# Kernel optimization log

Hardware: AMD Instinct MI355X
Metric: run time of the kernel (lower is better)

The kernel has to match this reference:

```python
import jax, jax.numpy as jnp
import numpy as np

D_MODEL = 512
NHEAD = 8
WINDOW = 64


def setup_inputs() -> dict:
    key = jax.random.key(0)
    ks = jax.random.split(key, 5)
    d = D_MODEL
    x = jax.random.normal(ks[0], (8, 2048, d), dtype=jnp.float32)
    # nn.MultiheadAttention params: packed in-proj [3d, d] + bias [3d], out-proj [d, d] + bias [d]
    scale = 1.0 / np.sqrt(d)
    in_proj_w = jax.random.normal(ks[1], (3 * d, d), dtype=jnp.float32) * scale
    in_proj_b = jnp.zeros((3 * d,), dtype=jnp.float32)
    out_proj_w = jax.random.normal(ks[2], (d, d), dtype=jnp.float32) * scale
    out_proj_b = jnp.zeros((d,), dtype=jnp.float32)
    return {"x": x, "in_proj_w": in_proj_w, "in_proj_b": in_proj_b,
            "out_proj_w": out_proj_w, "out_proj_b": out_proj_b}


def reference(x, in_proj_w, in_proj_b, out_proj_w, out_proj_b):
    B, L, d = x.shape
    H = NHEAD
    dh = d // H
    # packed qkv projection (torch Linear: x @ W.T + b)
    qkv = jnp.einsum('bld,ed->ble', x, in_proj_w) + in_proj_b  # [B, L, 3d]
    q, k, v = jnp.split(qkv, 3, axis=-1)
    # split heads -> [B, H, L, dh]
    def heads(t):
        return t.reshape(B, L, H, dh).transpose(0, 2, 1, 3)
    q, k, v = heads(q), heads(k), heads(v)
    scores = jnp.einsum('bhqd,bhkd->bhqk', q, k) / jnp.sqrt(jnp.float32(dh))
    # banded mask: positions with |i-j| > window are masked out
    idx = jnp.arange(L)
    band = jnp.abs(idx[None, :] - idx[:, None]) > WINDOW  # [L, L] bool
    scores = jnp.where(band[None, None, :, :], jnp.float32(-jnp.inf), scores)
    p = jax.nn.softmax(scores, axis=-1)
    out = jnp.einsum('bhqk,bhkd->bhqd', p, v)  # [B, H, L, dh]
    out = out.transpose(0, 2, 1, 3).reshape(B, L, d)
    return jnp.einsum('bld,ed->ble', out, out_proj_w) + out_proj_b
```

## Files before the change

kernel.cpp:

```cpp
#include <hip/hip_runtime.h>

typedef __bf16 bf16x8 __attribute__((ext_vector_type(8)));
typedef unsigned short u16;
typedef unsigned short u16x8 __attribute__((ext_vector_type(8)));
typedef float f32x4 __attribute__((ext_vector_type(4)));

#define L_SEQ 2048
#define NQT   (L_SEQ / 128)

__device__ __forceinline__ float bf2f(u16 x) {
    unsigned u = ((unsigned)x) << 16;
    return __builtin_bit_cast(float, u);
}
__device__ __forceinline__ u16 f2bf(float f) {
    unsigned u = __builtin_bit_cast(unsigned, f);
    u += 0x7FFFu + ((u >> 16) & 1u);
    return (u16)(u >> 16);
}

__device__ __forceinline__ void gload_lds16(const u16* g, u16* l) {
    __builtin_amdgcn_global_load_lds(
        (const __attribute__((address_space(1))) void*)g,
        (__attribute__((address_space(3))) void*)l, 16, 0, 0);
}

__global__ void cvt_all(const float* __restrict__ x, const float* __restrict__ wi,
                        const float* __restrict__ wo, u16* __restrict__ xo,
                        u16* __restrict__ wio, u16* __restrict__ woo,
                        int nx8, int nwi8, int nwo8) {
    int i = blockIdx.x * blockDim.x + threadIdx.x;
    const float* src; u16* dst;
    if (i < nx8) { src = x; dst = xo; }
    else if (i < nx8 + nwi8) { i -= nx8; src = wi; dst = wio; }
    else if (i < nx8 + nwi8 + nwo8) { i -= nx8 + nwi8; src = wo; dst = woo; }
    else return;
    const float4* p = reinterpret_cast<const float4*>(src) + (size_t)i * 2;
    const float4 a = p[0], b = p[1];
    u16x8 r;
    r[0] = f2bf(a.x); r[1] = f2bf(a.y); r[2] = f2bf(a.z); r[3] = f2bf(a.w);
    r[4] = f2bf(b.x); r[5] = f2bf(b.y); r[6] = f2bf(b.z); r[7] = f2bf(b.w);
    *(reinterpret_cast<u16x8*>(dst) + i) = r;
}

__launch_bounds__(512, 4)
__global__ void gemm_qkv(const u16* __restrict__ A, const u16* __restrict__ W,
                         const float* __restrict__ bias, u16* __restrict__ C,
                         int M, int N, int K) {
    __shared__ u16 As[3][256 * 32];
    __shared__ u16 Bs[3][128 * 32];

    const int tid   = threadIdx.x;
    const int lane  = tid & 63;
    const int wid   = tid >> 6;
    const int wm    = wid >> 1;
    const int wn    = wid & 1;
    const int row_l = lane & 15;
    const int grp   = lane >> 4;

    const int nwg  = gridDim.x * gridDim.y;
    const int hw   = blockIdx.y * gridDim.x + blockIdx.x;
    const int tile = (hw & 7) * (nwg >> 3) + (hw >> 3);
    const int m0 = (tile / gridDim.x) * 256;
    const int n0 = (tile % gridDim.x) * 128;

    const int srow = tid >> 2;
    const int scol = ((tid & 3) ^ ((tid >> 3) & 3)) * 8;
    const u16* gA = A + (size_t)(m0 + srow) * K + scol;
    const u16* gB = W + (size_t)(n0 + srow) * K + scol;

    f32x4 acc[4][4];
#pragma unroll
    for (int mi = 0; mi < 4; ++mi)
#pragma unroll
        for (int ni = 0; ni < 4; ++ni)
            acc[mi][ni] = (f32x4){0.f, 0.f, 0.f, 0.f};

    auto stage = [&](int buf, int kt) {
        gload_lds16(gA + (size_t)kt * 32,                   &As[buf][0]    + wid * 512);
        gload_lds16(gA + (size_t)128 * K + (size_t)kt * 32, &As[buf][4096] + wid * 512);
        gload_lds16(gB + (size_t)kt * 32,                   &Bs[buf][0]    + wid * 512);
    };

    const int rchunk = (grp ^ ((row_l >> 1) & 3)) * 8;

    const int NT = K >> 5;
    stage(0, 0);
    stage(1, 1);
    asm volatile("s_waitcnt vmcnt(3)" ::: "memory");
    __builtin_amdgcn_s_barrier();

    int buf = 0;
    for (int kt = 0; kt < NT; ++kt) {
        bf16x8 a[4], b[4];
#pragma unroll
        for (int mi = 0; mi < 4; ++mi)
            a[mi] = *reinterpret_cast<const bf16x8*>(
                &As[buf][(wm * 64 + mi * 16 + row_l) * 32 + rchunk]);
#pragma unroll
        for (int ni = 0; ni < 4; ++ni)
            b[ni] = *reinterpret_cast<const bf16x8*>(
                &Bs[buf][(wn * 64 + ni * 16 + row_l) * 32 + rchunk]);

        if (kt + 2 < NT) {
            int st = buf + 2; if (st >= 3) st -= 3;
            stage(st, kt + 2);
        }
        if (kt < NT - 2)       asm volatile("s_waitcnt vmcnt(3)" ::: "memory");
        else if (kt == NT - 2) asm volatile("s_waitcnt vmcnt(0)" ::: "memory");
        __builtin_amdgcn_s_barrier();
        asm volatile("s_waitcnt lgkmcnt(0)" ::: "memory");
        __builtin_amdgcn_sched_barrier(0);
        __builtin_amdgcn_s_setprio(1);
#pragma unroll
        for (int mi = 0; mi < 4; ++mi)
#pragma unroll
            for (int ni = 0; ni < 4; ++ni)
                acc[mi][ni] = __builtin_amdgcn_mfma_f32_16x16x32_bf16(a[mi], b[ni], acc[mi][ni], 0, 0, 0);
        __builtin_amdgcn_s_setprio(0);
        __builtin_amdgcn_s_barrier();
        buf = buf + 1; if (buf >= 3) buf = 0;
    }

#pragma unroll
    for (int ni = 0; ni < 4; ++ni) {
        const int col = n0 + wn * 64 + ni * 16 + row_l;
        const float bsf = bias[col];
#pragma unroll
        for (int mi = 0; mi < 4; ++mi) {
#pragma unroll
            for (int r = 0; r < 4; ++r) {
                const int rowm = m0 + wm * 64 + mi * 16 + grp * 4 + r;
                C[(size_t)rowm * N + col] = f2bf(acc[mi][ni][r] + bsf);
            }
        }
    }
}

template <bool OUT_BF16>
__launch_bounds__(256, 3)
__global__ void gemm_ring(const u16* __restrict__ A, const u16* __restrict__ W,
                          const float* __restrict__ bias, void* __restrict__ Cv,
                          int M, int N, int K) {
    __shared__ u16 As[3][128 * 32];
    __shared__ u16 Bs[3][128 * 32];

    const int tid   = threadIdx.x;
    const int lane  = tid & 63;
    const int wid   = tid >> 6;
    const int wm    = wid >> 1;
    const int wn    = wid & 1;
    const int row_l = lane & 15;
    const int grp   = lane >> 4;

    const int nwg  = gridDim.x * gridDim.y;
    const int hw   = blockIdx.y * gridDim.x + blockIdx.x;
    const int tile = (hw & 7) * (nwg >> 3) + (hw >> 3);
    const int m0 = (tile / gridDim.x) * 128;
    const int n0 = (tile % gridDim.x) * 128;

    const int srow = tid >> 2;
    const int scol = ((tid & 3) ^ ((tid >> 3) & 3)) * 8;
    const u16* gA = A + (size_t)(m0 + srow) * K + scol;
    const u16* gB = W + (size_t)(n0 + srow) * K + scol;

    f32x4 acc[4][4];
#pragma unroll
    for (int mi = 0; mi < 4; ++mi)
#pragma unroll
        for (int ni = 0; ni < 4; ++ni)
            acc[mi][ni] = (f32x4){0.f, 0.f, 0.f, 0.f};

    auto stage = [&](int buf, int kt) {
#pragma unroll
        for (int i = 0; i < 2; ++i) {
            gload_lds16(gA + (size_t)(i * 64) * K + kt * 32, &As[buf][i * 2048 + wid * 512]);
            gload_lds16(gB + (size_t)(i * 64) * K + kt * 32, &Bs[buf][i * 2048 + wid * 512]);
        }
    };

    const int rchunk = (grp ^ ((row_l >> 1) & 3)) * 8;

    auto compute = [&](int buf) {
        bf16x8 a[4], b[4];
#pragma unroll
        for (int mi = 0; mi < 4; ++mi)
            a[mi] = *reinterpret_cast<const bf16x8*>(
                &As[buf][(wm * 64 + mi * 16 + row_l) * 32 + rchunk]);
#pragma unroll
        for (int ni = 0; ni < 4; ++ni)
            b[ni] = *reinterpret_cast<const bf16x8*>(
                &Bs[buf][(wn * 64 + ni * 16 + row_l) * 32 + rchunk]);
        __builtin_amdgcn_s_setprio(1);
#pragma unroll
        for (int mi = 0; mi < 4; ++mi)
#pragma unroll
            for (int ni = 0; ni < 4; ++ni)
                acc[mi][ni] = __builtin_amdgcn_mfma_f32_16x16x32_bf16(a[mi], b[ni], acc[mi][ni], 0, 0, 0);
        __builtin_amdgcn_s_setprio(0);
    };

    const int NT = K >> 5;
    stage(0, 0);
    stage(1, 1);
    int cur = 0;
    for (int t = 0; t < NT; ++t) {
        if (t == NT - 1) asm volatile("s_waitcnt vmcnt(0)" ::: "memory");
        else             asm volatile("s_waitcnt vmcnt(4)" ::: "memory");
        __builtin_amdgcn_s_barrier();
        if (t + 2 < NT) {
            int st = cur + 2; if (st >= 3) st -= 3;
            stage(st, t + 2);
        }
        compute(cur);
        cur = cur + 1; if (cur >= 3) cur = 0;
    }

#pragma unroll
    for (int ni = 0; ni < 4; ++ni) {
        const int col = n0 + wn * 64 + ni * 16 + row_l;
        const float bsf = bias[col];
#pragma unroll
        for (int mi = 0; mi < 4; ++mi) {
#pragma unroll
            for (int r = 0; r < 4; ++r) {
                const int rowm = m0 + wm * 64 + mi * 16 + grp * 4 + r;
                const float v = acc[mi][ni][r] + bsf;
                if (OUT_BF16)
                    ((u16*)Cv)[(size_t)rowm * N + col] = f2bf(v);
                else
                    ((float*)Cv)[(size_t)rowm * N + col] = v;
            }
        }
    }
}

__launch_bounds__(512, 4)
__global__ void local_attn(const u16* __restrict__ qkv, u16* __restrict__ att) {
    __shared__ __align__(16) u16 Ks[256 * 64];
    __shared__ __align__(16) u16 Vt[64 * 256];
    __shared__ __align__(16) u16 Pl[8][512];

    const int tid   = threadIdx.x;
    const int lane  = tid & 63;
    const int wv    = tid >> 6;
    const int row_l = lane & 15;
    const int grp   = lane >> 4;
    const int qt = blockIdx.x, h = blockIdx.y, b = blockIdx.z;
    const int q0b = qt * 128;
    const int kstart = q0b - 64;
    const size_t base = (size_t)b * L_SEQ * 1536;
    const bool edge = (qt == 0) || (qt == NQT - 1);

    {
        const int r0 = tid >> 3;
        const int c  = tid & 7;
#pragma unroll
        for (int i = 0; i < 4; ++i) {
            const int row  = i * 64 + r0;
            const int keyg = min(max(kstart + row, 0), L_SEQ - 1);
            const int cg   = c ^ (row & 7);
            gload_lds16(qkv + base + (size_t)keyg * 1536 + 512 + h * 64 + cg * 8,
                        &Ks[i * 4096 + wv * 512]);
        }
    }
    {
#pragma unroll
        for (int i = 0; i < 4; ++i) {
            const int idx  = i * 512 + tid;
            const int row  = idx >> 3;
            const int c8   = idx & 7;
            const int keyg = min(max(kstart + row, 0), L_SEQ - 1);
            const u16x8 vu = *reinterpret_cast<const u16x8*>(
                qkv + base + (size_t)keyg * 1536 + 1024 + h * 64 + c8 * 8);
#pragma unroll
            for (int e = 0; e < 8; ++e) {
                const int d = c8 * 8 + e;
                const int slot = (row >> 3) ^ (d & 7) ^ ((d >> 3) & 7);
                Vt[d * 256 + slot * 8 + (row & 7)] = vu[e];
            }
        }
    }

    const int qrow_g = q0b + wv * 16 + row_l;
    const u16* qp = qkv + base + (size_t)qrow_g * 1536 + h * 64;
    const bf16x8 qf0 = *reinterpret_cast<const bf16x8*>(qp + grp * 8);
    const bf16x8 qf1 = *reinterpret_cast<const bf16x8*>(qp + 32 + grp * 8);

    __syncthreads();

    float m_r = -1e30f, l_r = 0.f;
    f32x4 acc[4];
#pragma unroll
    for (int ds = 0; ds < 4; ++ds) acc[ds] = (f32x4){0.f, 0.f, 0.f, 0.f};
    u16* Pw = Pl[wv];

    auto do_chunk = [&](int c, bool bandLo, bool bandHi, bool half, bool rng) {
        const int kcL = wv * 16 + 32 * c;
        const int kcG = kstart + kcL;
        const int nf = half ? 1 : 2;

        f32x4 s[2];
#pragma unroll
        for (int f = 0; f < 2; ++f) {
            if (f >= nf) break;
            const int rr = kcL + 16 * f + row_l;
            const bf16x8 ka = *reinterpret_cast<const bf16x8*>(
                &Ks[rr * 64 + ((grp ^ (rr & 7)) * 8)]);
            const bf16x8 kb = *reinterpret_cast<const bf16x8*>(
                &Ks[rr * 64 + (((grp + 4) ^ (rr & 7)) * 8)]);
            f32x4 z = (f32x4){0.f, 0.f, 0.f, 0.f};
            z = __builtin_amdgcn_mfma_f32_16x16x32_bf16(ka, qf0, z, 0, 0, 0);
            z = __builtin_amdgcn_mfma_f32_16x16x32_bf16(kb, qf1, z, 0, 0, 0);
            s[f] = z;
        }

        float p[2][4];
        float cmax = -1e30f;
#pragma unroll
        for (int f = 0; f < 2; ++f) {
            if (f >= nf) break;
#pragma unroll
            for (int r = 0; r < 4; ++r) {
                const int k = 16 * f + grp * 4 + r;
                bool ok = true;
                if (bandLo) ok = ok && (k >= row_l);
                if (bandHi) ok = ok && (k <= row_l);
                if (rng) { const int kg = kcG + k; ok = ok && (kg >= 0) && (kg < L_SEQ); }
                const float sv = ok ? s[f][r] * 0.125f : -1e30f;
                p[f][r] = sv;
                cmax = fmaxf(cmax, sv);
            }
        }
        cmax = fmaxf(cmax, __shfl_xor(cmax, 16, 64));
        cmax = fmaxf(cmax, __shfl_xor(cmax, 32, 64));

        const bool need = !__all(cmax <= m_r + 8.f);
        float mu;
        float scl = 1.f;
        if (need) {
            const float mn = fmaxf(m_r, cmax);
            scl = __expf(m_r - mn);
            m_r = mn;
            mu  = mn;
        } else {
            mu = m_r;
        }

        float lsum = 0.f;
#pragma unroll
        for (int f = 0; f < 2; ++f) {
            if (f >= nf) break;
#pragma unroll
            for (int r = 0; r < 4; ++r) {
                const float pv = (p[f][r] <= -1e29f) ? 0.f : __expf(p[f][r] - mu);
                p[f][r] = pv;
                lsum += pv;
            }
        }
        lsum += __shfl_xor(lsum, 16, 64);
        lsum += __shfl_xor(lsum, 32, 64);
        l_r = l_r * scl + lsum;

        if (need) {
            float scl4[4];
#pragma unroll
            for (int r = 0; r < 4; ++r) scl4[r] = __shfl(scl, grp * 4 + r, 64);
#pragma unroll
            for (int ds = 0; ds < 4; ++ds)
#pragma unroll
                for (int r = 0; r < 4; ++r) acc[ds][r] *= scl4[r];
        }

#pragma unroll
        for (int f = 0; f < 2; ++f)
#pragma unroll
            for (int r = 0; r < 4; ++r) {
                const int k = 16 * f + grp * 4 + r;
                const int slot = (k >> 3) ^ ((row_l >> 1) & 3);
                const float pv = (f < nf) ? p[f][r] : 0.f;
                Pw[row_l * 32 + slot * 8 + (k & 7)] = f2bf(pv);
            }
        const bf16x8 pa = *reinterpret_cast<const bf16x8*>(
            &Pw[row_l * 32 + ((grp ^ ((row_l >> 1) & 3)) * 8)]);

        int k0 = kcL + grp * 8;
        if (half) k0 = min(k0, 248);
#pragma unroll
        for (int ds = 0; ds < 4; ++ds) {
            const int d = ds * 16 + row_l;
            const int slot = (k0 >> 3) ^ (d & 7) ^ ((d >> 3) & 7);
            const bf16x8 vf = *reinterpret_cast<const bf16x8*>(
                &Vt[d * 256 + slot * 8]);
            acc[ds] = __builtin_amdgcn_mfma_f32_16x16x32_bf16(pa, vf, acc[ds], 0, 0, 0);
        }
    };

    if (!edge) {
        do_chunk(0, true,  false, false, false);
        do_chunk(1, false, false, false, false);
        do_chunk(2, false, false, false, false);
        do_chunk(3, false, false, false, false);
        do_chunk(4, false, true,  true,  false);
    } else {
        const int kw = kstart + wv * 16;
        if (kw       > -32 && kw       < L_SEQ) do_chunk(0, true,  false, false, true);
        if (kw + 32  > -32 && kw + 32  < L_SEQ) do_chunk(1, false, false, false, true);
        if (kw + 64  > -32 && kw + 64  < L_SEQ) do_chunk(2, false, false, false, true);
        if (kw + 96  > -32 && kw + 96  < L_SEQ) do_chunk(3, false, false, false, true);
        if (kw + 128 > -32 && kw + 128 < L_SEQ) do_chunk(4, false, true,  true,  true);
    }

    const float inv = 1.f / l_r;
    float inv4[4];
#pragma unroll
    for (int r = 0; r < 4; ++r) inv4[r] = __shfl(inv, grp * 4 + r, 64);
    const int qg = q0b + wv * 16 + grp * 4;
#pragma unroll
    for (int r = 0; r < 4; ++r)
#pragma unroll
        for (int ds = 0; ds < 4; ++ds)
            att[(size_t)(b * L_SEQ + qg + r) * 512 + h * 64 + ds * 16 + row_l] =
                f2bf(acc[ds][r] * inv4[r]);
}

extern "C" void kernel_launch(void* const* d_in, const int* in_sizes, int n_in,
                              void* d_out, int out_size, void* d_ws, size_t ws_size,
                              hipStream_t stream) {
    const float* x     = (const float*)d_in[0];
    const float* w_in  = (const float*)d_in[1];
    const float* b_in  = (const float*)d_in[2];
    const float* w_out = (const float*)d_in[3];
    const float* b_out = (const float*)d_in[4];
    float* out = (float*)d_out;

    const int B = 8, L = L_SEQ;
    const int M = B * L;

    u16* qkv   = (u16*)d_ws;
    u16* att   = qkv   + (size_t)M * 1536;
    u16* x_bf  = att   + (size_t)M * 512;
    u16* wi_bf = x_bf  + (size_t)M * 512;
    u16* wo_bf = wi_bf + (size_t)1536 * 512;

    const int nx8  = M * 512 / 8;
    const int nwi8 = 1536 * 512 / 8;
    const int nwo8 = 512 * 512 / 8;
    const int ncvt = nx8 + nwi8 + nwo8;
    cvt_all<<<(ncvt + 255) / 256, 256, 0, stream>>>(x, w_in, w_out, x_bf, wi_bf, wo_bf,
                                                    nx8, nwi8, nwo8);

    gemm_qkv<<<dim3(1536 / 128, M / 256), dim3(512), 0, stream>>>(
        x_bf, wi_bf, b_in, qkv, M, 1536, 512);

    local_attn<<<dim3(NQT, 8, B), dim3(512), 0, stream>>>(qkv, att);

    gemm_ring<false><<<dim3(512 / 128, M / 128), dim3(256), 0, stream>>>(
        att, wo_bf, b_out, out, M, 512, 512);
}
```

Measured before the change: 86.90 us.

## Fuse fp32-to-bf16 conversion of x into the QKV GEMM A-tile load

Drops the separate pass that converts activations x to bf16 and instead has the QKV GEMM read fp32 x directly into registers, convert, and write swizzled bf16 into LDS, with a restructured register-prefetch pipeline for A while B keeps async global-to-LDS loads. This removes a full write and re-read of the bf16 copy of x. In exchange, each GEMM block reads twice the A bytes, and since x is reused across 12 N-tiles the extra global traffic may offset the saved conversion kernel. A-tile staging now goes through VGPRs, which adds register pressure and a barrier each iteration.

```diff
diff --git a/kernel.cpp b/kernel.cpp
--- a/kernel.cpp
+++ b/kernel.cpp
@@ -7,6 +7,7 @@
 
 #define L_SEQ 2048
 #define NQT   (L_SEQ / 128)
+#define SB()  __builtin_amdgcn_sched_barrier(0)
 
 __device__ __forceinline__ float bf2f(u16 x) {
     unsigned u = ((unsigned)x) << 16;
@@ -24,15 +25,13 @@
         (__attribute__((address_space(3))) void*)l, 16, 0, 0);
 }
 
-__global__ void cvt_all(const float* __restrict__ x, const float* __restrict__ wi,
-                        const float* __restrict__ wo, u16* __restrict__ xo,
-                        u16* __restrict__ wio, u16* __restrict__ woo,
-                        int nx8, int nwi8, int nwo8) {
+__global__ void cvt_w(const float* __restrict__ wi, const float* __restrict__ wo,
+                      u16* __restrict__ wio, u16* __restrict__ woo,
+                      int nwi8, int nwo8) {
     int i = blockIdx.x * blockDim.x + threadIdx.x;
     const float* src; u16* dst;
-    if (i < nx8) { src = x; dst = xo; }
-    else if (i < nx8 + nwi8) { i -= nx8; src = wi; dst = wio; }
-    else if (i < nx8 + nwi8 + nwo8) { i -= nx8 + nwi8; src = wo; dst = woo; }
+    if (i < nwi8) { src = wi; dst = wio; }
+    else if (i < nwi8 + nwo8) { i -= nwi8; src = wo; dst = woo; }
     else return;
     const float4* p = reinterpret_cast<const float4*>(src) + (size_t)i * 2;
     const float4 a = p[0], b = p[1];
@@ -43,7 +42,7 @@
 }
 
 __launch_bounds__(512, 4)
-__global__ void gemm_qkv(const u16* __restrict__ A, const u16* __restrict__ W,
+__global__ void gemm_qkv(const float* __restrict__ A, const u16* __restrict__ W,
                          const float* __restrict__ bias, u16* __restrict__ C,
                          int M, int N, int K) {
     __shared__ u16 As[3][256 * 32];
@@ -63,10 +62,16 @@
     const int m0 = (tile / gridDim.x) * 256;
     const int n0 = (tile % gridDim.x) * 128;
 
-    const int srow = tid >> 2;
-    const int scol = ((tid & 3) ^ ((tid >> 3) & 3)) * 8;
-    const u16* gA = A + (size_t)(m0 + srow) * K + scol;
-    const u16* gB = W + (size_t)(n0 + srow) * K + scol;
+    const int arow = tid >> 1;
+    const int av   = (arow >> 1) & 3;
+    const int g0   = ((tid & 1) * 2)     ^ av;
+    const int g1   = ((tid & 1) * 2 + 1) ^ av;
+    const float* gA0 = A + (size_t)(m0 + arow) * K + g0 * 8;
+    const float* gA1 = A + (size_t)(m0 + arow) * K + g1 * 8;
+
+    const int brow = tid >> 2;
+    const int bcol = ((tid & 3) ^ ((tid >> 3) & 3)) * 8;
+    const u16* gB = W + (size_t)(n0 + brow) * K + bcol;
 
     f32x4 acc[4][4];
 #pragma unroll
@@ -75,22 +80,35 @@
         for (int ni = 0; ni < 4; ++ni)
             acc[mi][ni] = (f32x4){0.f, 0.f, 0.f, 0.f};
 
-    auto stage = [&](int buf, int kt) {
-        gload_lds16(gA + (size_t)kt * 32,                   &As[buf][0]    + wid * 512);
-        gload_lds16(gA + (size_t)128 * K + (size_t)kt * 32, &As[buf][4096] + wid * 512);
-        gload_lds16(gB + (size_t)kt * 32,                   &Bs[buf][0]    + wid * 512);
-    };
-
     const int rchunk = (grp ^ ((row_l >> 1) & 3)) * 8;
-
     const int NT = K >> 5;
-    stage(0, 0);
-    stage(1, 1);
-    asm volatile("s_waitcnt vmcnt(3)" ::: "memory");
-    __builtin_amdgcn_s_barrier();
+
+    {
+        const f32x4* q0 = reinterpret_cast<const f32x4*>(gA0);
+        const f32x4* q1 = reinterpret_cast<const f32x4*>(gA1);
+        f32x4 p00 = q0[0], p01 = q0[1], p10 = q1[0], p11 = q1[1];
+        SB();
+        gload_lds16(gB,      &Bs[0][0] + wid * 512);
+        SB();
+        gload_lds16(gB + 32, &Bs[1][0] + wid * 512);
+        SB();
+        asm volatile("s_waitcnt vmcnt(2)" ::: "memory");
+        SB();
+        u16x8 w0, w1;
+#pragma unroll
+        for (int e = 0; e < 4; ++e) {
+            w0[e] = f2bf(p00[e]); w0[4 + e] = f2bf(p01[e]);
+            w1[e] = f2bf(p10[e]); w1[4 + e] = f2bf(p11[e]);
+        }
+        *reinterpret_cast<u16x8*>(&As[0][(2 * tid + 0) * 8]) = w0;
+        *reinterpret_cast<u16x8*>(&As[0][(2 * tid + 1) * 8]) = w1;
+        asm volatile("s_waitcnt vmcnt(1)" ::: "memory");
+        asm volatile("s_waitcnt lgkmcnt(0)" ::: "memory");
+        __builtin_amdgcn_s_barrier();
+    }
 
     int buf = 0;
-    for (int kt = 0; kt < NT; ++kt) {
+    for (int t = 0; t < NT; ++t) {
         bf16x8 a[4], b[4];
 #pragma unroll
         for (int mi = 0; mi < 4; ++mi)
@@ -100,16 +118,21 @@
         for (int ni = 0; ni < 4; ++ni)
             b[ni] = *reinterpret_cast<const bf16x8*>(
                 &Bs[buf][(wn * 64 + ni * 16 + row_l) * 32 + rchunk]);
-
-        if (kt + 2 < NT) {
-            int st = buf + 2; if (st >= 3) st -= 3;
-            stage(st, kt + 2);
-        }
-        if (kt < NT - 2)       asm volatile("s_waitcnt vmcnt(3)" ::: "memory");
-        else if (kt == NT - 2) asm volatile("s_waitcnt vmcnt(0)" ::: "memory");
-        __builtin_amdgcn_s_barrier();
+        SB();
+        f32x4 p00, p01, p10, p11;
+        if (t + 1 < NT) {
+            const f32x4* q0 = reinterpret_cast<const f32x4*>(gA0 + (t + 1) * 32);
+            const f32x4* q1 = reinterpret_cast<const f32x4*>(gA1 + (t + 1) * 32);
+            p00 = q0[0]; p01 = q0[1]; p10 = q1[0]; p11 = q1[1];
+        }
+        SB();
+        if (t + 2 < NT) {
+            int sb = buf + 2; if (sb >= 3) sb -= 3;
+            gload_lds16(gB + (size_t)(t + 2) * 32, &Bs[sb][0] + wid * 512);
+        }
+        SB();
         asm volatile("s_waitcnt lgkmcnt(0)" ::: "memory");
-        __builtin_amdgcn_sched_barrier(0);
+        SB();
         __builtin_amdgcn_s_setprio(1);
 #pragma unroll
         for (int mi = 0; mi < 4; ++mi)
@@ -117,7 +140,23 @@
             for (int ni = 0; ni < 4; ++ni)
                 acc[mi][ni] = __builtin_amdgcn_mfma_f32_16x16x32_bf16(a[mi], b[ni], acc[mi][ni], 0, 0, 0);
         __builtin_amdgcn_s_setprio(0);
-        __builtin_amdgcn_s_barrier();
+        SB();
+        if (t + 1 < NT) {
+            if (t + 2 < NT) asm volatile("s_waitcnt vmcnt(1)" ::: "memory");
+            else            asm volatile("s_waitcnt vmcnt(0)" ::: "memory");
+            SB();
+            int wb = buf + 1; if (wb >= 3) wb -= 3;
+            u16x8 w0, w1;
+#pragma unroll
+            for (int e = 0; e < 4; ++e) {
+                w0[e] = f2bf(p00[e]); w0[4 + e] = f2bf(p01[e]);
+                w1[e] = f2bf(p10[e]); w1[4 + e] = f2bf(p11[e]);
+            }
+            *reinterpret_cast<u16x8*>(&As[wb][(2 * tid + 0) * 8]) = w0;
+            *reinterpret_cast<u16x8*>(&As[wb][(2 * tid + 1) * 8]) = w1;
+            asm volatile("s_waitcnt lgkmcnt(0)" ::: "memory");
+            __builtin_amdgcn_s_barrier();
+        }
         buf = buf + 1; if (buf >= 3) buf = 0;
     }
 
@@ -438,19 +477,16 @@
 
     u16* qkv   = (u16*)d_ws;
     u16* att   = qkv   + (size_t)M * 1536;
-    u16* x_bf  = att   + (size_t)M * 512;
-    u16* wi_bf = x_bf  + (size_t)M * 512;
+    u16* wi_bf = att   + (size_t)M * 512;
     u16* wo_bf = wi_bf + (size_t)1536 * 512;
 
-    const int nx8  = M * 512 / 8;
     const int nwi8 = 1536 * 512 / 8;
     const int nwo8 = 512 * 512 / 8;
-    const int ncvt = nx8 + nwi8 + nwo8;
-    cvt_all<<<(ncvt + 255) / 256, 256, 0, stream>>>(x, w_in, w_out, x_bf, wi_bf, wo_bf,
-                                                    nx8, nwi8, nwo8);
+    const int ncvt = nwi8 + nwo8;
+    cvt_w<<<(ncvt + 255) / 256, 256, 0, stream>>>(w_in, w_out, wi_bf, wo_bf, nwi8, nwo8);
 
     gemm_qkv<<<dim3(1536 / 128, M / 256), dim3(512), 0, stream>>>(
-        x_bf, wi_bf, b_in, qkv, M, 1536, 512);
+        x, wi_bf, b_in, qkv, M, 1536, 512);
 
     local_attn<<<dim3(NQT, 8, B), dim3(512), 0, stream>>>(qkv, att);
 
```

After: 102.3 us. 17.7% more time.
